# Kernel tuning notes

Measured on AMD Instinct MI355X. Metric: run time of the kernel, lower is better.

## Reference

```python
import jax, jax.numpy as jnp
import numpy as np

N, C, H, W = 32, 512, 32, 32
D = C // 2  # theta/phi embed channels


def setup_inputs() -> dict:
    key = jax.random.key(0)
    ks = jax.random.split(key, 7)
    s = 0.05
    return {
        "x": jax.random.normal(ks[0], (N, C, H, W), jnp.float32),
        "W_theta": jax.random.normal(ks[1], (D, C), jnp.float32) * s,
        "b_theta": jax.random.normal(ks[2], (D,), jnp.float32) * s,
        "W_phi": jax.random.normal(ks[3], (D, C), jnp.float32) * s,
        "b_phi": jax.random.normal(ks[4], (D,), jnp.float32) * s,
        "W_fuse": jax.random.normal(ks[5], (C, C), jnp.float32) * s,
        "b_fuse": jax.random.normal(ks[6], (C,), jnp.float32) * s,
    }


def _conv1x1(x, Wt, bt):
    # 1x1 conv == per-pixel linear: [n,c,h,w] x [o,c] -> [n,o,h,w]
    return jnp.einsum('nchw,oc->nohw', x, Wt) + bt[None, :, None, None]


def reference(x, W_theta, b_theta, W_phi, b_phi, W_fuse, b_fuse):
    n, c, h, w = x.shape
    theta = _conv1x1(x, W_theta, b_theta)          # [n, d, h, w]
    phi = _conv1x1(x, W_phi, b_phi)                # [n, d, h, w]
    d = theta.shape[1]
    hw = h * w
    t = theta.reshape(n, d, hw)                    # queries [n, d, hw]
    p = phi.reshape(n, d, hw)                      # keys    [n, d, hw]
    g = x.reshape(n, c, hw)                        # values  [n, c, hw]
    scale = 1.0 / np.sqrt(float(d))
    f = jnp.einsum('ndq,ndk->nqk', t, p) * scale   # [n, hw, hw]
    f = jax.nn.softmax(f, axis=-1)
    attn = jnp.einsum('nqk,nck->ncq', f, g).reshape(n, c, h, w)
    return x + _conv1x1(attn, W_fuse, b_fuse)
```

## Files before the change

kernel.cpp:

```cpp
#include <hip/hip_runtime.h>


#define NB  32
#define CC  512
#define HWD 1024

typedef __attribute__((ext_vector_type(8))) short short8;
typedef __attribute__((ext_vector_type(4))) float f32x4;

__device__ __forceinline__ unsigned short f2bu(float f) {
    unsigned int u = __float_as_uint(f);
    u = (u + 0x7FFFu + ((u >> 16) & 1u)) >> 16;
    return (unsigned short)u;
}

__global__ __launch_bounds__(256) void k_packw(const float* __restrict__ Wt,
                                               const float* __restrict__ Wp,
                                               const float* __restrict__ Wf,
                                               unsigned short* __restrict__ Wcat,
                                               unsigned short* __restrict__ Wfuse) {
    int idx = blockIdx.x * 256 + threadIdx.x;
    int o = idx >> 9;
    float cv = (o < 256) ? Wt[idx] : Wp[idx - 131072];
    Wcat[idx]  = f2bu(cv);
    Wfuse[idx] = f2bu(Wf[idx]);
}

__global__ __launch_bounds__(512) void k_mm(const float* __restrict__ x,
                                            const unsigned short* __restrict__ Wcat,
                                            const unsigned short* __restrict__ Wfuse,
                                            const float* __restrict__ bt,
                                            const float* __restrict__ bp,
                                            unsigned short* __restrict__ tp,
                                            unsigned short* __restrict__ Z) {
    __shared__ __align__(16) float Tr[32 * 132];
    __shared__ __align__(16) unsigned short As[128 * 40];
    __shared__ __align__(16) unsigned short Bs[256 * 40];
    const int m0 = blockIdx.x << 7;
    const int yb = blockIdx.y;
    const bool isZ = (yb >= 2);
    const int n0 = (yb & 1) << 8;
    const unsigned short* W = isZ ? Wfuse : Wcat;
    const int n  = m0 >> 10, qbase = m0 & 1023;
    const int t = threadIdx.x, lane = t & 63, wave = t >> 6;
    const int wr = wave >> 2, wc = wave & 3;
    const int lrow = lane & 15, hi = lane >> 4, lhk = hi << 3;
    const f32x4 fz = {0.f, 0.f, 0.f, 0.f};
    f32x4 acc[4][4];
#pragma unroll
    for (int i = 0; i < 4; ++i)
#pragma unroll
        for (int j = 0; j < 4; ++j) acc[i][j] = fz;

    const int tr_r = t >> 4, tr_q = (t & 15) << 3;
    const int p2_pix = t & 127, p2_c = (t >> 7) << 3;

    for (int kt = 0; kt < 16; ++kt) {
        const int k0 = kt << 5;
        {
            const float* src = x + ((size_t)(n * CC + k0 + tr_r)) * HWD + qbase + tr_q;
            float4 v0 = *(const float4*)(src);
            float4 v1 = *(const float4*)(src + 4);
            *(float4*)(Tr + tr_r * 132 + tr_q) = v0;
            *(float4*)(Tr + tr_r * 132 + tr_q + 4) = v1;
#pragma unroll
            for (int i = 0; i < 2; ++i) {
                int chunk = t + (i << 9);
                int r = chunk >> 2, ko = (chunk & 3) << 3;
                *(uint4*)(Bs + r * 40 + ko) =
                    *(const uint4*)(W + ((size_t)(n0 + r)) * CC + k0 + ko);
            }
        }
        __syncthreads();
        {
            short8 o8;
#pragma unroll
            for (int j = 0; j < 8; ++j)
                o8[j] = (short)f2bu(Tr[(p2_c + j) * 132 + p2_pix]);
            *(short8*)(As + p2_pix * 40 + p2_c) = o8;
        }
        __syncthreads();
        short8 af[4], bfm[4];
#pragma unroll
        for (int mi = 0; mi < 4; ++mi)
            af[mi] = *(const short8*)(As + (wr * 64 + mi * 16 + lrow) * 40 + lhk);
#pragma unroll
        for (int ni = 0; ni < 4; ++ni)
            bfm[ni] = *(const short8*)(Bs + (wc * 64 + ni * 16 + lrow) * 40 + lhk);
#pragma unroll
        for (int mi = 0; mi < 4; ++mi)
#pragma unroll
            for (int ni = 0; ni < 4; ++ni)
                acc[mi][ni] = __builtin_amdgcn_mfma_f32_16x16x32_bf16(
                    af[mi], bfm[ni], acc[mi][ni], 0, 0, 0);
        __syncthreads();
    }
    if (!isZ) {
#pragma unroll
        for (int ni = 0; ni < 4; ++ni) {
            const int col = n0 + wc * 64 + ni * 16 + lrow;
            const float bias = (col < 256) ? bt[col] : bp[col - 256];
#pragma unroll
            for (int mi = 0; mi < 4; ++mi)
#pragma unroll
                for (int j = 0; j < 4; ++j) {
                    const int row = m0 + wr * 64 + mi * 16 + hi * 4 + j;
                    tp[(size_t)row * CC + col] = f2bu(acc[mi][ni][j] + bias);
                }
        }
    } else {
        const int kbase = qbase + wr * 64;
        unsigned short* Zn = Z + (size_t)n * CC * HWD;
#pragma unroll
        for (int ni = 0; ni < 4; ++ni) {
            const int o = n0 + wc * 64 + ni * 16 + lrow;
#pragma unroll
            for (int mi = 0; mi < 4; ++mi) {
                ushort4 v;
                v.x = f2bu(acc[mi][ni][0]);
                v.y = f2bu(acc[mi][ni][1]);
                v.z = f2bu(acc[mi][ni][2]);
                v.w = f2bu(acc[mi][ni][3]);
                *(ushort4*)(Zn + (size_t)o * HWD + kbase + mi * 16 + (hi << 2)) = v;
            }
        }
    }
}

__global__ __launch_bounds__(512, 2) void k_attn7(const unsigned short* __restrict__ tp,
                                                  const unsigned short* __restrict__ Z,
                                                  const float* __restrict__ bfu,
                                                  const float* __restrict__ x,
                                                  float* __restrict__ out) {
    constexpr int QST = 264;
    constexpr int PST = 264;
    constexpr int QSZ = 64 * QST;
    __shared__ __align__(16) unsigned short SL[QSZ + 64 * PST];
    __shared__ float rowsum[64];
    unsigned short* Qs = SL;
    unsigned short* P  = SL + QSZ;

    const int b = blockIdx.x;
    const int n = (b & 15) | ((b >> 8) << 4);
    const int q0 = ((b >> 4) & 15) << 6;
    const int t = threadIdx.x, lane = t & 63, wave = t >> 6;
    const int lrow = lane & 15, hi = lane >> 4, lhk = hi << 3;
    const f32x4 fz = {0.f, 0.f, 0.f, 0.f};

    const unsigned short* tpn = tp + (size_t)n * HWD * CC;
    const unsigned short* Zn  = Z + (size_t)n * CC * HWD;

    if (t < 64) rowsum[t] = 0.f;
#pragma unroll
    for (int pass = 0; pass < 4; ++pass) {
        int chunk = (pass << 9) + t;
        int row = chunk >> 5, co = (chunk & 31) << 3;
        *(short8*)(Qs + row * QST + co) =
            *(const short8*)(tpn + (size_t)(q0 + row) * CC + co);
    }
    __syncthreads();

    f32x4 accF[4][4];
#pragma unroll
    for (int mi = 0; mi < 4; ++mi)
#pragma unroll
        for (int qj = 0; qj < 4; ++qj) accF[mi][qj] = fz;
    float psum[4][4];
#pragma unroll
    for (int qj = 0; qj < 4; ++qj)
#pragma unroll
        for (int j = 0; j < 4; ++j) psum[qj][j] = 0.f;

    const int kw = wave << 4;
    const int ob = wave << 6;

    for (int it = 0; it < 4; ++it) {
        const int kv0 = it << 8;
        const size_t krow0 = (size_t)(kv0 + kw + lrow) * CC + 256;
        const size_t krow1 = (size_t)(kv0 + 128 + kw + lrow) * CC + 256;
        f32x4 accA[2][4];
#pragma unroll
        for (int k2 = 0; k2 < 2; ++k2)
#pragma unroll
            for (int qj = 0; qj < 4; ++qj) accA[k2][qj] = fz;
        short8 kpre[2][2];
        kpre[0][0] = *(const short8*)(tpn + krow0 + lhk);
        kpre[0][1] = *(const short8*)(tpn + krow1 + lhk);
#pragma unroll
        for (int kt = 0; kt < 8; ++kt) {
            const int d0 = (kt << 5) + lhk;
            if (kt < 7) {
                const int dn = ((kt + 1) << 5) + lhk;
                kpre[(kt + 1) & 1][0] = *(const short8*)(tpn + krow0 + dn);
                kpre[(kt + 1) & 1][1] = *(const short8*)(tpn + krow1 + dn);
            }
            short8 qfr[4];
#pragma unroll
            for (int qj = 0; qj < 4; ++qj)
                qfr[qj] = *(const short8*)(Qs + (qj * 16 + lrow) * QST + d0);
            __builtin_amdgcn_s_setprio(1);
#pragma unroll
            for (int k2 = 0; k2 < 2; ++k2)
#pragma unroll
                for (int qj = 0; qj < 4; ++qj)
                    accA[k2][qj] = __builtin_amdgcn_mfma_f32_16x16x32_bf16(
                        qfr[qj], kpre[kt & 1][k2], accA[k2][qj], 0, 0, 0);
            __builtin_amdgcn_s_setprio(0);
        }
#pragma unroll
        for (int k2 = 0; k2 < 2; ++k2) {
            const int pcol = (k2 << 7) + kw + lrow;
#pragma unroll
            for (int qj = 0; qj < 4; ++qj)
#pragma unroll
                for (int j = 0; j < 4; ++j) {
                    float p = __expf(accA[k2][qj][j] * 0.0625f);
                    psum[qj][j] += p;
                    P[(qj * 16 + hi * 4 + j) * PST + pcol] = f2bu(p);
                }
        }
        __syncthreads();
        short8 zfr[3][4];
#pragma unroll
        for (int s = 0; s < 2; ++s)
#pragma unroll
            for (int mi = 0; mi < 4; ++mi)
                zfr[s][mi] = *(const short8*)(Zn + (size_t)(ob + mi * 16 + lrow) * HWD +
                                              kv0 + (s << 5) + lhk);
        __builtin_amdgcn_s_setprio(1);
#pragma unroll
        for (int ks = 0; ks < 8; ++ks) {
            const int kb = (ks << 5) + lhk;
            if (ks < 6) {
#pragma unroll
                for (int mi = 0; mi < 4; ++mi)
                    zfr[(ks + 2) % 3][mi] =
                        *(const short8*)(Zn + (size_t)(ob + mi * 16 + lrow) * HWD +
                                         kv0 + ((ks + 2) << 5) + lhk);
            }
#pragma unroll
            for (int qj = 0; qj < 4; ++qj) {
                short8 pa = *(const short8*)(P + (qj * 16 + lrow) * PST + kb);
#pragma unroll
                for (int mi = 0; mi < 4; ++mi)
                    accF[mi][qj] = __builtin_amdgcn_mfma_f32_16x16x32_bf16(
                        zfr[ks % 3][mi], pa, accF[mi][qj], 0, 0, 0);
            }
        }
        __builtin_amdgcn_s_setprio(0);
        __syncthreads();
    }

#pragma unroll
    for (int qj = 0; qj < 4; ++qj)
#pragma unroll
        for (int j = 0; j < 4; ++j) {
            float s = psum[qj][j];
            s += __shfl_xor(s, 1, 16);
            s += __shfl_xor(s, 2, 16);
            s += __shfl_xor(s, 4, 16);
            s += __shfl_xor(s, 8, 16);
            if (lrow == 0) atomicAdd(&rowsum[qj * 16 + hi * 4 + j], s);
        }
    __syncthreads();

    float inv[4];
#pragma unroll
    for (int qj = 0; qj < 4; ++qj) inv[qj] = 1.f / rowsum[qj * 16 + lrow];
#pragma unroll
    for (int mi = 0; mi < 4; ++mi) {
#pragma unroll
        for (int j = 0; j < 4; ++j) {
            const int o = ob + mi * 16 + hi * 4 + j;
            const float bias = bfu[o];
#pragma unroll
            for (int qj = 0; qj < 4; ++qj) {
                const int q = q0 + qj * 16 + lrow;
                const size_t idx = ((size_t)(n * CC + o)) * HWD + q;
                out[idx] = accF[mi][qj][j] * inv[qj] + bias + x[idx];
            }
        }
    }
}

extern "C" void kernel_launch(void* const* d_in, const int* in_sizes, int n_in,
                              void* d_out, int out_size, void* d_ws, size_t ws_size,
                              hipStream_t stream) {
    const float* x  = (const float*)d_in[0];
    const float* Wt = (const float*)d_in[1];
    const float* bt = (const float*)d_in[2];
    const float* Wp = (const float*)d_in[3];
    const float* bp = (const float*)d_in[4];
    const float* Wf = (const float*)d_in[5];
    const float* bfu = (const float*)d_in[6];
    float* out = (float*)d_out;

    char* ws = (char*)d_ws;
    unsigned short* tp    = (unsigned short*)(ws);
    unsigned short* Z     = (unsigned short*)(ws + 33554432);
    unsigned short* Wcat  = (unsigned short*)(ws + 67108864);
    unsigned short* Wfuse = (unsigned short*)(ws + 67633152);

    k_packw<<<dim3(1024), 256, 0, stream>>>(Wt, Wp, Wf, Wcat, Wfuse);
    k_mm   <<<dim3(256, 4), 512, 0, stream>>>(x, Wcat, Wfuse, bt, bp, tp, Z);
    k_attn7<<<dim3(512), 512, 0, stream>>>(tp, Z, bfu, x, out);
}
```

Baseline: 190.6 us.

## Double query tile to 128 rows per attention block and vectorize epilogue

Each attention block now processes 128 query rows instead of 64, halving the grid to 256 blocks. The goal is to reuse each loaded K and Z fragment across twice as many queries, cutting global reads of tp and Z. The MFMA operands are swapped so the output accumulates with queries along the contiguous axis, which allows float4 loads of x and float4 stores of out. Register software prefetch is dropped and the row-sum reduction moves inside the loop. The larger accumulators (accG 8x4 plus accA 2x8) and doubled LDS raise register and LDS pressure. 256 blocks may also underfill the GPU's compute units.

```diff
diff --git a/kernel.cpp b/kernel.cpp
--- a/kernel.cpp
+++ b/kernel.cpp
@@ -127,22 +127,22 @@
     }
 }
 
-__global__ __launch_bounds__(512, 2) void k_attn7(const unsigned short* __restrict__ tp,
+__global__ __launch_bounds__(512, 2) void k_attn8(const unsigned short* __restrict__ tp,
                                                   const unsigned short* __restrict__ Z,
                                                   const float* __restrict__ bfu,
                                                   const float* __restrict__ x,
                                                   float* __restrict__ out) {
     constexpr int QST = 264;
     constexpr int PST = 264;
-    constexpr int QSZ = 64 * QST;
-    __shared__ __align__(16) unsigned short SL[QSZ + 64 * PST];
-    __shared__ float rowsum[64];
+    constexpr int QSZ = 128 * QST;
+    __shared__ __align__(16) unsigned short SL[QSZ + 128 * PST];
+    __shared__ float rowsum[128];
     unsigned short* Qs = SL;
     unsigned short* P  = SL + QSZ;
 
     const int b = blockIdx.x;
-    const int n = (b & 15) | ((b >> 8) << 4);
-    const int q0 = ((b >> 4) & 15) << 6;
+    const int n = b & 31;
+    const int q0 = (b >> 5) << 7;
     const int t = threadIdx.x, lane = t & 63, wave = t >> 6;
     const int lrow = lane & 15, hi = lane >> 4, lhk = hi << 3;
     const f32x4 fz = {0.f, 0.f, 0.f, 0.f};
@@ -150,9 +150,9 @@
     const unsigned short* tpn = tp + (size_t)n * HWD * CC;
     const unsigned short* Zn  = Z + (size_t)n * CC * HWD;
 
-    if (t < 64) rowsum[t] = 0.f;
-#pragma unroll
-    for (int pass = 0; pass < 4; ++pass) {
+    if (t < 128) rowsum[t] = 0.f;
+#pragma unroll
+    for (int pass = 0; pass < 8; ++pass) {
         int chunk = (pass << 9) + t;
         int row = chunk >> 5, co = (chunk & 31) << 3;
         *(short8*)(Qs + row * QST + co) =
@@ -160,16 +160,11 @@
     }
     __syncthreads();
 
-    f32x4 accF[4][4];
-#pragma unroll
-    for (int mi = 0; mi < 4; ++mi)
-#pragma unroll
-        for (int qj = 0; qj < 4; ++qj) accF[mi][qj] = fz;
-    float psum[4][4];
-#pragma unroll
-    for (int qj = 0; qj < 4; ++qj)
-#pragma unroll
-        for (int j = 0; j < 4; ++j) psum[qj][j] = 0.f;
+    f32x4 accG[8][4];
+#pragma unroll
+    for (int qj = 0; qj < 8; ++qj)
+#pragma unroll
+        for (int mi = 0; mi < 4; ++mi) accG[qj][mi] = fz;
 
     const int kw = wave << 4;
     const int ob = wave << 6;
@@ -178,40 +173,33 @@
         const int kv0 = it << 8;
         const size_t krow0 = (size_t)(kv0 + kw + lrow) * CC + 256;
         const size_t krow1 = (size_t)(kv0 + 128 + kw + lrow) * CC + 256;
-        f32x4 accA[2][4];
+        f32x4 accA[2][8];
 #pragma unroll
         for (int k2 = 0; k2 < 2; ++k2)
 #pragma unroll
-            for (int qj = 0; qj < 4; ++qj) accA[k2][qj] = fz;
-        short8 kpre[2][2];
-        kpre[0][0] = *(const short8*)(tpn + krow0 + lhk);
-        kpre[0][1] = *(const short8*)(tpn + krow1 + lhk);
+            for (int qj = 0; qj < 8; ++qj) accA[k2][qj] = fz;
 #pragma unroll
         for (int kt = 0; kt < 8; ++kt) {
             const int d0 = (kt << 5) + lhk;
-            if (kt < 7) {
-                const int dn = ((kt + 1) << 5) + lhk;
-                kpre[(kt + 1) & 1][0] = *(const short8*)(tpn + krow0 + dn);
-                kpre[(kt + 1) & 1][1] = *(const short8*)(tpn + krow1 + dn);
-            }
-            short8 qfr[4];
-#pragma unroll
-            for (int qj = 0; qj < 4; ++qj)
-                qfr[qj] = *(const short8*)(Qs + (qj * 16 + lrow) * QST + d0);
-            __builtin_amdgcn_s_setprio(1);
-#pragma unroll
-            for (int k2 = 0; k2 < 2; ++k2)
-#pragma unroll
-                for (int qj = 0; qj < 4; ++qj)
-                    accA[k2][qj] = __builtin_amdgcn_mfma_f32_16x16x32_bf16(
-                        qfr[qj], kpre[kt & 1][k2], accA[k2][qj], 0, 0, 0);
-            __builtin_amdgcn_s_setprio(0);
-        }
+            short8 kf0 = *(const short8*)(tpn + krow0 + d0);
+            short8 kf1 = *(const short8*)(tpn + krow1 + d0);
+#pragma unroll
+            for (int qj = 0; qj < 8; ++qj) {
+                short8 qfr = *(const short8*)(Qs + (qj * 16 + lrow) * QST + d0);
+                accA[0][qj] = __builtin_amdgcn_mfma_f32_16x16x32_bf16(qfr, kf0, accA[0][qj], 0, 0, 0);
+                accA[1][qj] = __builtin_amdgcn_mfma_f32_16x16x32_bf16(qfr, kf1, accA[1][qj], 0, 0, 0);
+            }
+        }
+        float psum[8][4];
+#pragma unroll
+        for (int qj = 0; qj < 8; ++qj)
+#pragma unroll
+            for (int j = 0; j < 4; ++j) psum[qj][j] = 0.f;
 #pragma unroll
         for (int k2 = 0; k2 < 2; ++k2) {
             const int pcol = (k2 << 7) + kw + lrow;
 #pragma unroll
-            for (int qj = 0; qj < 4; ++qj)
+            for (int qj = 0; qj < 8; ++qj)
 #pragma unroll
                 for (int j = 0; j < 4; ++j) {
                     float p = __expf(accA[k2][qj][j] * 0.0625f);
@@ -219,66 +207,58 @@
                     P[(qj * 16 + hi * 4 + j) * PST + pcol] = f2bu(p);
                 }
         }
-        __syncthreads();
-        short8 zfr[3][4];
-#pragma unroll
-        for (int s = 0; s < 2; ++s)
-#pragma unroll
-            for (int mi = 0; mi < 4; ++mi)
-                zfr[s][mi] = *(const short8*)(Zn + (size_t)(ob + mi * 16 + lrow) * HWD +
-                                              kv0 + (s << 5) + lhk);
+#pragma unroll
+        for (int qj = 0; qj < 8; ++qj)
+#pragma unroll
+            for (int j = 0; j < 4; ++j) {
+                float s = psum[qj][j];
+                s += __shfl_xor(s, 1, 16);
+                s += __shfl_xor(s, 2, 16);
+                s += __shfl_xor(s, 4, 16);
+                s += __shfl_xor(s, 8, 16);
+                if (lrow == 0) atomicAdd(&rowsum[qj * 16 + hi * 4 + j], s);
+            }
+        __syncthreads();
         __builtin_amdgcn_s_setprio(1);
 #pragma unroll
         for (int ks = 0; ks < 8; ++ks) {
             const int kb = (ks << 5) + lhk;
-            if (ks < 6) {
+            short8 zf[4];
+#pragma unroll
+            for (int mi = 0; mi < 4; ++mi)
+                zf[mi] = *(const short8*)(Zn + (size_t)(ob + mi * 16 + lrow) * HWD + kv0 + kb);
+#pragma unroll
+            for (int qj = 0; qj < 8; ++qj) {
+                short8 pa = *(const short8*)(P + (qj * 16 + lrow) * PST + kb);
 #pragma unroll
                 for (int mi = 0; mi < 4; ++mi)
-                    zfr[(ks + 2) % 3][mi] =
-                        *(const short8*)(Zn + (size_t)(ob + mi * 16 + lrow) * HWD +
-                                         kv0 + ((ks + 2) << 5) + lhk);
-            }
-#pragma unroll
-            for (int qj = 0; qj < 4; ++qj) {
-                short8 pa = *(const short8*)(P + (qj * 16 + lrow) * PST + kb);
-#pragma unroll
-                for (int mi = 0; mi < 4; ++mi)
-                    accF[mi][qj] = __builtin_amdgcn_mfma_f32_16x16x32_bf16(
-                        zfr[ks % 3][mi], pa, accF[mi][qj], 0, 0, 0);
+                    accG[qj][mi] = __builtin_amdgcn_mfma_f32_16x16x32_bf16(
+                        pa, zf[mi], accG[qj][mi], 0, 0, 0);
             }
         }
         __builtin_amdgcn_s_setprio(0);
         __syncthreads();
     }
 
-#pragma unroll
-    for (int qj = 0; qj < 4; ++qj)
-#pragma unroll
-        for (int j = 0; j < 4; ++j) {
-            float s = psum[qj][j];
-            s += __shfl_xor(s, 1, 16);
-            s += __shfl_xor(s, 2, 16);
-            s += __shfl_xor(s, 4, 16);
-            s += __shfl_xor(s, 8, 16);
-            if (lrow == 0) atomicAdd(&rowsum[qj * 16 + hi * 4 + j], s);
-        }
+    if (t < 128) rowsum[t] = 1.f / rowsum[t];
     __syncthreads();
-
-    float inv[4];
-#pragma unroll
-    for (int qj = 0; qj < 4; ++qj) inv[qj] = 1.f / rowsum[qj * 16 + lrow];
-#pragma unroll
-    for (int mi = 0; mi < 4; ++mi) {
-#pragma unroll
-        for (int j = 0; j < 4; ++j) {
-            const int o = ob + mi * 16 + hi * 4 + j;
-            const float bias = bfu[o];
-#pragma unroll
-            for (int qj = 0; qj < 4; ++qj) {
-                const int q = q0 + qj * 16 + lrow;
-                const size_t idx = ((size_t)(n * CC + o)) * HWD + q;
-                out[idx] = accF[mi][qj][j] * inv[qj] + bias + x[idx];
-            }
+    float bias[4];
+#pragma unroll
+    for (int mi = 0; mi < 4; ++mi) bias[mi] = bfu[ob + mi * 16 + lrow];
+#pragma unroll
+    for (int qj = 0; qj < 8; ++qj) {
+        const float4 inv4 = *(const float4*)&rowsum[qj * 16 + (hi << 2)];
+#pragma unroll
+        for (int mi = 0; mi < 4; ++mi) {
+            const int o = ob + mi * 16 + lrow;
+            const size_t idx = ((size_t)(n * CC + o)) * HWD + q0 + qj * 16 + (hi << 2);
+            const float4 xr = *(const float4*)(x + idx);
+            float4 r;
+            r.x = accG[qj][mi][0] * inv4.x + bias[mi] + xr.x;
+            r.y = accG[qj][mi][1] * inv4.y + bias[mi] + xr.y;
+            r.z = accG[qj][mi][2] * inv4.z + bias[mi] + xr.z;
+            r.w = accG[qj][mi][3] * inv4.w + bias[mi] + xr.w;
+            *(float4*)(out + idx) = r;
         }
     }
 }
@@ -303,5 +283,5 @@
 
     k_packw<<<dim3(1024), 256, 0, stream>>>(Wt, Wp, Wf, Wcat, Wfuse);
     k_mm   <<<dim3(256, 4), 512, 0, stream>>>(x, Wcat, Wfuse, bt, bp, tp, Z);
-    k_attn7<<<dim3(512), 512, 0, stream>>>(tp, Z, bfu, x, out);
-}
+    k_attn8<<<dim3(256), 512, 0, stream>>>(tp, Z, bfu, x, out);
+}
```

Result: faster. 170.4 us, median of 3 (-10.6%).
